# Performance work log

Hardware: AMD Instinct MI355X
Metric: run time of the kernel (lower is better)

The kernel has to match this reference:

```python
import jax, jax.numpy as jnp
import numpy as np

T, B, E, H = 2048, 2, 1024, 16
D = E // H  # head_dim = 64

def setup_inputs() -> dict:
    key = jax.random.key(0)
    ks = jax.random.split(key, 9)
    s = 1.0 / np.sqrt(E)
    return {
        "query": jax.random.normal(ks[0], (T, B, E), dtype=jnp.float32),
        "Wq": jax.random.normal(ks[1], (E, E), dtype=jnp.float32) * s,
        "bq": jax.random.normal(ks[2], (E,), dtype=jnp.float32) * 0.02,
        "Wk": jax.random.normal(ks[3], (E, E), dtype=jnp.float32) * s,
        "bk": jax.random.normal(ks[4], (E,), dtype=jnp.float32) * 0.02,
        "Wv": jax.random.normal(ks[5], (E, E), dtype=jnp.float32) * s,
        "bv": jax.random.normal(ks[6], (E,), dtype=jnp.float32) * 0.02,
        "Wo": jax.random.normal(ks[7], (E, E), dtype=jnp.float32) * s,
        "bo": jax.random.normal(ks[8], (E,), dtype=jnp.float32) * 0.02,
    }

def reference(query, Wq, bq, Wk, bk, Wv, bv, Wo, bo):
    # query: [T, B, E] (fairseq Time x Batch x Channel layout)
    t, b, e = query.shape
    scaling = D ** -0.5
    q = (query @ Wq.T + bq) * scaling          # [T,B,E], scaled like fairseq
    k = query @ Wk.T + bk                      # self-attention: k,v from query
    v = query @ Wv.T + bv
    # split heads: [T,B,H,D]
    q = q.reshape(t, b, H, D)
    k = k.reshape(t, b, H, D)
    v = v.reshape(t, b, H, D)
    # attn weights: [B,H,T(tgt),S(src)]
    scores = jnp.einsum("tbhd,sbhd->bhts", q, k)
    probs = jax.nn.softmax(scores, axis=-1)
    # attend: [T,B,H,D] -> [T,B,E]
    ctx = jnp.einsum("bhts,sbhd->tbhd", probs, v).reshape(t, b, e)
    return ctx @ Wo.T + bo                     # [T,B,E]
```

## Files before the change

### kernel.cpp

```cpp
#include <hip/hip_runtime.h>
#include <hip/hip_bf16.h>
#include <math.h>

#define TT 2048
#define BB 2
#define EE 1024
#define HH 16
#define DD 64
#define RR (TT*BB)

typedef __bf16 bf16x8 __attribute__((ext_vector_type(8)));
typedef float  floatx4 __attribute__((ext_vector_type(4)));

__device__ __forceinline__ unsigned short f2b(float f) {
    union { float f; unsigned u; } x{f};
    return (unsigned short)((x.u + 0x7FFFu + ((x.u >> 16) & 1u)) >> 16);
}
__device__ __forceinline__ float b2f_lo(unsigned u) {
    union { unsigned u; float f; } x{u << 16}; return x.f;
}
__device__ __forceinline__ float b2f_hi(unsigned u) {
    union { unsigned u; float f; } x{u & 0xffff0000u}; return x.f;
}

__device__ __forceinline__ float exp2_fast(float x) {
    return __builtin_amdgcn_exp2f(x);
}

typedef const __attribute__((address_space(1))) unsigned int as1_u32;
typedef __attribute__((address_space(3))) unsigned int as3_u32;
__device__ __forceinline__ void gload16(const void* g, void* l) {
    __builtin_amdgcn_global_load_lds((as1_u32*)g, (as3_u32*)l, 16, 0, 0);
}

#define SCALE_Q 0.18033688011112042f

__device__ __forceinline__ int swz(int r) {
    return (r & 7) ^ (((r >> 3) & 3) << 1);
}

__global__ __launch_bounds__(256)
void pack_bf16(const float* __restrict__ x,  const float* __restrict__ wq,
               const float* __restrict__ wk, const float* __restrict__ wv,
               const float* __restrict__ wo, unsigned short* __restrict__ base,
               unsigned short* __restrict__ wob)
{
    const size_t M4 = (size_t)4 << 20, M7 = (size_t)7 << 20;
    const size_t e0 = ((size_t)blockIdx.x * 256 + threadIdx.x) * 8;
    const float* src;
    unsigned short* dst;
    if (e0 < M4) {
        src = x + e0; dst = base + e0;
    } else if (e0 < M7) {
        const int seg = (int)((e0 >> 20) - 4);
        const float* wsrc[3] = {wq, wk, wv};
        src = wsrc[seg] + (e0 & ((1u << 20) - 1));
        dst = base + e0;
    } else {
        src = wo + (e0 - M7); dst = wob + (e0 - M7);
    }
    const float4 a = *(const float4*)src;
    const float4 b = *(const float4*)(src + 4);
    union { unsigned short u[8]; uint4 v; } p;
    p.u[0] = f2b(a.x); p.u[1] = f2b(a.y); p.u[2] = f2b(a.z); p.u[3] = f2b(a.w);
    p.u[4] = f2b(b.x); p.u[5] = f2b(b.y); p.u[6] = f2b(b.z); p.u[7] = f2b(b.w);
    *(uint4*)dst = p.v;
}

template<int MODE>
__global__ __launch_bounds__(256)
void gemm_mfma(const unsigned short* __restrict__ A,
               const unsigned short* __restrict__ Bw,
               const float* __restrict__ b0, const float* __restrict__ b1,
               const float* __restrict__ b2,
               void* __restrict__ out0, void* __restrict__ out1,
               void* __restrict__ out2)
{
    constexpr int BM = 128;
    constexpr int BN = (MODE == 0) ? 128 : 64;
    constexpr int MT = 4;
    constexpr int NT = (MODE == 0) ? 4 : 2;
    constexpr int RA = BM / 32;
    constexpr int RB = BN / 32;
    constexpr int SMEM = (MODE == 0) ? 34816 : 24576;
    __shared__ __align__(16) unsigned char smem[SMEM];
    unsigned short* ldsA = (unsigned short*)smem;
    unsigned short* ldsB = (unsigned short*)(smem + BM * 128);

    const int tid  = threadIdx.x;
    const int w    = tid >> 6;
    const int lane = tid & 63;
    const int quad = lane >> 4;
    const int l15  = lane & 15;
    const int wm   = w & 1;
    const int wn   = w >> 1;
    const int i0   = blockIdx.x * BM;
    const int j0   = blockIdx.y * BN;

    const unsigned short* ga[RA];
    const unsigned short* gb[RB];
    #pragma unroll
    for (int r = 0; r < RA; ++r) {
        const int slot = r * 256 + tid;
        const int row  = slot >> 3;
        const int gc   = (slot & 7) ^ swz(row);
        ga[r] = A + (size_t)(i0 + row) * EE + gc * 8;
    }
    #pragma unroll
    for (int r = 0; r < RB; ++r) {
        const int slot = r * 256 + tid;
        const int row  = slot >> 3;
        const int gc   = (slot & 7) ^ swz(row);
        gb[r] = Bw + (size_t)(j0 + row) * EE + gc * 8;
    }

    int ofsA[2][MT], ofsB[2][NT];
    #pragma unroll
    for (int mt = 0; mt < MT; ++mt) {
        const int row = wm * 64 + mt * 16 + l15;
        #pragma unroll
        for (int ks = 0; ks < 2; ++ks)
            ofsA[ks][mt] = row * 64 + (((ks * 4 + quad) ^ swz(row)) << 3);
    }
    #pragma unroll
    for (int nt = 0; nt < NT; ++nt) {
        const int col = wn * (BN / 2) + nt * 16 + l15;
        #pragma unroll
        for (int ks = 0; ks < 2; ++ks)
            ofsB[ks][nt] = col * 64 + (((ks * 4 + quad) ^ swz(col)) << 3);
    }

    floatx4 acc[MT][NT];
    #pragma unroll
    for (int mt = 0; mt < MT; ++mt)
        #pragma unroll
        for (int nt = 0; nt < NT; ++nt)
            acc[mt][nt] = (floatx4){0.f, 0.f, 0.f, 0.f};

    for (int kk = 0; kk < EE; kk += 64) {
        __syncthreads();
        #pragma unroll
        for (int r = 0; r < RA; ++r)
            gload16(ga[r] + kk, ldsA + (r * 256 + w * 64) * 8);
        #pragma unroll
        for (int r = 0; r < RB; ++r)
            gload16(gb[r] + kk, ldsB + (r * 256 + w * 64) * 8);
        __syncthreads();

        #pragma unroll
        for (int ks = 0; ks < 2; ++ks) {
            bf16x8 af[MT], bfr[NT];
            #pragma unroll
            for (int mt = 0; mt < MT; ++mt)
                af[mt] = __builtin_bit_cast(bf16x8, *(const uint4*)&ldsA[ofsA[ks][mt]]);
            #pragma unroll
            for (int nt = 0; nt < NT; ++nt)
                bfr[nt] = __builtin_bit_cast(bf16x8, *(const uint4*)&ldsB[ofsB[ks][nt]]);
            #pragma unroll
            for (int mt = 0; mt < MT; ++mt)
                #pragma unroll
                for (int nt = 0; nt < NT; ++nt)
                    acc[mt][nt] = __builtin_amdgcn_mfma_f32_16x16x32_bf16(
                        af[mt], bfr[nt], acc[mt][nt], 0, 0, 0);
        }
    }

    if (MODE == 1) {
        float* dst = (float*)out0;
        #pragma unroll
        for (int nt = 0; nt < NT; ++nt) {
            const int j = j0 + wn * 32 + nt * 16 + l15;
            const float bb = b0[j];
            #pragma unroll
            for (int mt = 0; mt < MT; ++mt) {
                const int i = i0 + wm * 64 + mt * 16 + quad * 4;
                #pragma unroll
                for (int r2 = 0; r2 < 4; ++r2)
                    dst[(size_t)(i + r2) * EE + j] = acc[mt][nt][r2] + bb;
            }
        }
    } else {
        const int which = j0 >> 10;
        const float scale = (which == 0) ? SCALE_Q : 1.0f;
        const float* bias = (which == 0) ? b0 : (which == 1) ? b1 : b2;
        if (which < 2) {
            unsigned short* dst = (unsigned short*)(which == 0 ? out0 : out1);
            #pragma unroll
            for (int nt = 0; nt < NT; ++nt) {
                const int j = (j0 & 1023) + wn * 64 + nt * 16 + l15;
                const int h = j >> 6, d = j & 63;
                const float bb = bias[j];
                #pragma unroll
                for (int mt = 0; mt < MT; ++mt) {
                    const int i = i0 + wm * 64 + mt * 16 + quad * 4;
                    #pragma unroll
                    for (int r2 = 0; r2 < 4; ++r2) {
                        const int ii = i + r2;
                        const int t = ii >> 1, b = ii & 1;
                        dst[((size_t)(b * HH + h) * TT + t) * DD + d] =
                            f2b((acc[mt][nt][r2] + bb) * scale);
                    }
                }
            }
        } else {
            __syncthreads();
            unsigned short* tr = (unsigned short*)smem + (size_t)w * 64 * 68;
            #pragma unroll
            for (int nt = 0; nt < NT; ++nt) {
                const int jl = nt * 16 + l15;
                const float bb = bias[(j0 & 1023) + wn * 64 + jl];
                #pragma unroll
                for (int mt = 0; mt < MT; ++mt) {
                    const int il0 = mt * 16 + quad * 4;
                    ushort4 h4;
                    h4.x = f2b(acc[mt][nt][0] + bb);
                    h4.y = f2b(acc[mt][nt][1] + bb);
                    h4.z = f2b(acc[mt][nt][2] + bb);
                    h4.w = f2b(acc[mt][nt][3] + bb);
                    *(ushort4*)&tr[jl * 68 + il0] = h4;
                }
            }
            __syncthreads();
            const int jg = (j0 & 1023) + wn * 64 + lane;
            const int h = jg >> 6, d = jg & 63;
            const int tb = (i0 + wm * 64) >> 1;
            const unsigned short* rp = tr + (size_t)lane * 68;
            unsigned short* dstV = (unsigned short*)out2;
            #pragma unroll
            for (int g = 0; g < 4; ++g) {
                union { unsigned short u[8]; uint4 v; } pe, po;
                #pragma unroll
                for (int k = 0; k < 8; ++k) {
                    pe.u[k] = rp[(g * 8 + k) * 2];
                    po.u[k] = rp[(g * 8 + k) * 2 + 1];
                }
                *(uint4*)&dstV[((size_t)(0 * HH + h) * DD + d) * TT + tb + g * 8] = pe.v;
                *(uint4*)&dstV[((size_t)(1 * HH + h) * DD + d) * TT + tb + g * 8] = po.v;
            }
        }
    }
}

__global__ __launch_bounds__(256)
void attn_mfma(const unsigned short* __restrict__ Q,
               const unsigned short* __restrict__ K,
               const unsigned short* __restrict__ Vt,
               unsigned short* __restrict__ cpart,
               float* __restrict__ lsumbuf)
{
    __shared__ __align__(16) unsigned short ksm[2][64 * 64];
    __shared__ __align__(16) unsigned short vtm[2][64 * 64];

    const int tid  = threadIdx.x;
    const int w    = tid >> 6;
    const int lane = tid & 63;
    const int quad = lane >> 4;
    const int l15  = lane & 15;
    const int bh   = blockIdx.x;
    const int tt   = blockIdx.y;
    const int half = blockIdx.z;

    const unsigned short* Qh = Q  + (size_t)bh * TT * DD;
    const unsigned short* Kh = K  + (size_t)bh * TT * DD;
    const unsigned short* Vh = Vt + (size_t)bh * DD * TT;

    const int q0w  = tt * 128 + w * 32;
    const int key0 = half * 1024;

    bf16x8 qf[2][2];
    #pragma unroll
    for (int qn = 0; qn < 2; ++qn)
        #pragma unroll
        for (int kd = 0; kd < 2; ++kd)
            qf[qn][kd] = __builtin_bit_cast(bf16x8,
                *(const uint4*)&Qh[(size_t)(q0w + qn * 16 + l15) * DD + kd * 32 + quad * 8]);

    const unsigned short* kg[4];
    #pragma unroll
    for (int r = 0; r < 4; ++r) {
        const int slot = r * 256 + tid;
        const int row  = slot >> 3;
        const int gc   = (slot & 7) ^ swz(row);
        kg[r] = Kh + (size_t)(key0 + row) * DD + gc * 8;
    }
    const unsigned short* vg[4];
    #pragma unroll
    for (int r = 0; r < 4; ++r) {
        const int s512 = (r & 1) * 256 + tid;
        const int rowd = s512 >> 3;
        const int gc   = (s512 & 7) ^ swz(rowd);
        vg[r] = Vh + (size_t)rowd * TT + key0 + (r >> 1) * 64 + gc * 8;
    }

    int ofsKA[4][2], ofsVB[4][2];
    #pragma unroll
    for (int mt = 0; mt < 4; ++mt) {
        const int row = ((mt >> 1) << 5) + ((l15 >> 2) << 3) + ((mt & 1) << 2) + (l15 & 3);
        #pragma unroll
        for (int kd = 0; kd < 2; ++kd)
            ofsKA[mt][kd] = row * 64 + (((kd * 4 + quad) ^ swz(row)) << 3);
    }
    #pragma unroll
    for (int dn = 0; dn < 4; ++dn) {
        const int row = dn * 16 + l15;
        #pragma unroll
        for (int ks = 0; ks < 2; ++ks)
            ofsVB[dn][ks] = row * 64 + (((ks * 4 + quad) ^ swz(row)) << 3);
    }

    floatx4 cacc[4][2];
    #pragma unroll
    for (int dn = 0; dn < 4; ++dn)
        #pragma unroll
        for (int qn = 0; qn < 2; ++qn)
            cacc[dn][qn] = (floatx4){0.f, 0.f, 0.f, 0.f};
    float rs[2] = {0.f, 0.f};

    for (int big = 0; big < 8; ++big) {
        const size_t ko = (size_t)big * 128;
        __syncthreads();
        gload16(kg[0] + ko * DD, &ksm[0][(size_t)(0 * 256 + w * 64) * 8]);
        gload16(kg[1] + ko * DD, &ksm[0][(size_t)(1 * 256 + w * 64) * 8]);
        gload16(kg[2] + ko * DD, &ksm[1][(size_t)(0 * 256 + w * 64) * 8]);
        gload16(kg[3] + ko * DD, &ksm[1][(size_t)(1 * 256 + w * 64) * 8]);
        gload16(vg[0] + ko,      &vtm[0][(size_t)(0 * 256 + w * 64) * 8]);
        gload16(vg[1] + ko,      &vtm[0][(size_t)(1 * 256 + w * 64) * 8]);
        gload16(vg[2] + ko,      &vtm[1][(size_t)(0 * 256 + w * 64) * 8]);
        gload16(vg[3] + ko,      &vtm[1][(size_t)(1 * 256 + w * 64) * 8]);
        __syncthreads();

        #pragma unroll
        for (int sub = 0; sub < 2; ++sub) {
            uint2 pk[4][2];
            #pragma unroll
            for (int mt = 0; mt < 4; ++mt) {
                const bf16x8 ka0 = __builtin_bit_cast(bf16x8, *(const uint4*)&ksm[sub][ofsKA[mt][0]]);
                const bf16x8 ka1 = __builtin_bit_cast(bf16x8, *(const uint4*)&ksm[sub][ofsKA[mt][1]]);
                #pragma unroll
                for (int qn = 0; qn < 2; ++qn) {
                    floatx4 s = (floatx4){0.f, 0.f, 0.f, 0.f};
                    s = __builtin_amdgcn_mfma_f32_16x16x32_bf16(ka0, qf[qn][0], s, 0, 0, 0);
                    s = __builtin_amdgcn_mfma_f32_16x16x32_bf16(ka1, qf[qn][1], s, 0, 0, 0);
                    const float p0 = exp2_fast(s[0]);
                    const float p1 = exp2_fast(s[1]);
                    const float p2 = exp2_fast(s[2]);
                    const float p3 = exp2_fast(s[3]);
                    rs[qn] += (p0 + p1) + (p2 + p3);
                    union { __hip_bfloat162 h2[2]; uint2 u; } c;
                    c.h2[0] = __float22bfloat162_rn(make_float2(p0, p1));
                    c.h2[1] = __float22bfloat162_rn(make_float2(p2, p3));
                    pk[mt][qn] = c.u;
                }
            }
            bf16x8 pa[2][2];
            #pragma unroll
            for (int qn = 0; qn < 2; ++qn) {
                union { uint2 d[2]; uint4 v; } a0, a1;
                a0.d[0] = pk[0][qn]; a0.d[1] = pk[1][qn];
                a1.d[0] = pk[2][qn]; a1.d[1] = pk[3][qn];
                pa[qn][0] = __builtin_bit_cast(bf16x8, a0.v);
                pa[qn][1] = __builtin_bit_cast(bf16x8, a1.v);
            }
            #pragma unroll
            for (int dn = 0; dn < 4; ++dn) {
                const bf16x8 vb0 = __builtin_bit_cast(bf16x8, *(const uint4*)&vtm[sub][ofsVB[dn][0]]);
                const bf16x8 vb1 = __builtin_bit_cast(bf16x8, *(const uint4*)&vtm[sub][ofsVB[dn][1]]);
                #pragma unroll
                for (int qn = 0; qn < 2; ++qn) {
                    cacc[dn][qn] = __builtin_amdgcn_mfma_f32_16x16x32_bf16(pa[qn][0], vb0, cacc[dn][qn], 0, 0, 0);
                    cacc[dn][qn] = __builtin_amdgcn_mfma_f32_16x16x32_bf16(pa[qn][1], vb1, cacc[dn][qn], 0, 0, 0);
                }
            }
        }
    }

    const int b = bh / HH, hh = bh % HH;
    float rsw[2];
    #pragma unroll
    for (int qn = 0; qn < 2; ++qn) {
        float t = rs[qn];
        t += __shfl_xor(t, 16);
        t += __shfl_xor(t, 32);
        rsw[qn] = t;
    }
    unsigned short* cp = cpart + (size_t)half * RR * EE;
    #pragma unroll
    for (int qn = 0; qn < 2; ++qn) {
        #pragma unroll
        for (int dn = 0; dn < 4; ++dn) {
            const int e = hh * 64 + dn * 16 + l15;
            #pragma unroll
            for (int j = 0; j < 4; ++j) {
                const int t = q0w + qn * 16 + quad * 4 + j;
                cp[(size_t)(t * BB + b) * EE + e] = f2b(cacc[dn][qn][j]);
            }
        }
    }
    if (quad == 0) {
        lsumbuf[(half * BB * HH + bh) * TT + q0w + 0 * 16 + l15] = rsw[0];
        lsumbuf[(half * BB * HH + bh) * TT + q0w + 1 * 16 + l15] = rsw[1];
    }
}

__global__ __launch_bounds__(256)
void combine(const unsigned short* __restrict__ cpart,
             const float* __restrict__ lsumbuf,
             unsigned short* __restrict__ cb)
{
    const int gid = blockIdx.x * 256 + threadIdx.x;
    const int e0 = (gid & 127) * 8;
    const int r  = gid >> 7;
    const int t = r >> 1, b = r & 1;
    const int h = e0 >> 6;
    const int bh = b * HH + h;
    const float inv = 1.0f /
        (lsumbuf[bh * TT + t] + lsumbuf[(BB * HH + bh) * TT + t]);
    const uint4 c0 = *(const uint4*)&cpart[(size_t)r * EE + e0];
    const uint4 c1 = *(const uint4*)&cpart[(size_t)RR * EE + (size_t)r * EE + e0];
    const unsigned u0[4] = {c0.x, c0.y, c0.z, c0.w};
    const unsigned u1[4] = {c1.x, c1.y, c1.z, c1.w};
    union { unsigned u[4]; uint4 v; } o;
    #pragma unroll
    for (int k = 0; k < 4; ++k) {
        const float lo = (b2f_lo(u0[k]) + b2f_lo(u1[k])) * inv;
        const float hi = (b2f_hi(u0[k]) + b2f_hi(u1[k])) * inv;
        union { __hip_bfloat162 h2; unsigned u; } pk;
        pk.h2 = __float22bfloat162_rn(make_float2(lo, hi));
        o.u[k] = pk.u;
    }
    *(uint4*)&cb[(size_t)r * EE + e0] = o.v;
}

extern "C" void kernel_launch(void* const* d_in, const int* in_sizes, int n_in,
                              void* d_out, int out_size, void* d_ws, size_t ws_size,
                              hipStream_t stream)
{
    const float* x  = (const float*)d_in[0];
    const float* Wq = (const float*)d_in[1];
    const float* bq = (const float*)d_in[2];
    const float* Wk = (const float*)d_in[3];
    const float* bk = (const float*)d_in[4];
    const float* Wv = (const float*)d_in[5];
    const float* bv = (const float*)d_in[6];
    const float* Wo = (const float*)d_in[7];
    const float* bo = (const float*)d_in[8];
    float* out = (float*)d_out;

    const size_t M1 = (size_t)1 << 20;
    unsigned short* base  = (unsigned short*)d_ws;
    unsigned short* xb    = base;
    unsigned short* wqkv  = base + 4 * M1;
    unsigned short* cpart = base;
    unsigned short* qb    = base + 8 * M1;
    unsigned short* kb    = base + 12 * M1;
    unsigned short* vtb   = base + 16 * M1;
    unsigned short* cb    = base + 20 * M1;
    unsigned short* wob   = base + 24 * M1;
    float*          lsum  = (float*)(base + 25 * M1);

    dim3 blk(256);

    pack_bf16<<<dim3(4096), blk, 0, stream>>>(x, Wq, Wk, Wv, Wo, base, wob);

    gemm_mfma<0><<<dim3(RR / 128, 3072 / 128), blk, 0, stream>>>(
        xb, wqkv, bq, bk, bv, qb, kb, vtb);

    attn_mfma<<<dim3(BB * HH, TT / 128, 2), blk, 0, stream>>>(qb, kb, vtb, cpart, lsum);

    combine<<<dim3(RR * EE / 8 / 256), blk, 0, stream>>>(cpart, lsum, cb);

    gemm_mfma<1><<<dim3(RR / 128, EE / 64), blk, 0, stream>>>(
        cb, wob, bo, nullptr, nullptr, out, nullptr, nullptr);
}
```

Before: 196.8 us.

## Use single-wave attention blocks with fp16 P·V and per-wave K/V tiles

The attention kernel now runs one 64-lane wave per block over 32 queries, loading 32-key K/V tiles into its own small LDS buffers. This removes the block-wide __syncthreads and replaces them with a vmcnt wait. V is now stored as fp16 by the QKV GEMM, and probabilities are packed with cvt_pkrtz so the P·V product uses the f16 MFMA. The goal is cheaper packing and more resident blocks without barriers. The cost is that each block no longer shares K/V loads across waves, which multiplies global/L2 traffic, and the smaller tiles add per-iteration overhead with no load double-buffering.

```diff
diff --git a/kernel.cpp b/kernel.cpp
--- a/kernel.cpp
+++ b/kernel.cpp
@@ -9,12 +9,18 @@
 #define DD 64
 #define RR (TT*BB)
 
-typedef __bf16 bf16x8 __attribute__((ext_vector_type(8)));
-typedef float  floatx4 __attribute__((ext_vector_type(4)));
+typedef __bf16    bf16x8  __attribute__((ext_vector_type(8)));
+typedef _Float16  halfx8  __attribute__((ext_vector_type(8)));
+typedef _Float16  halfx2  __attribute__((ext_vector_type(2)));
+typedef float     floatx4 __attribute__((ext_vector_type(4)));
 
 __device__ __forceinline__ unsigned short f2b(float f) {
     union { float f; unsigned u; } x{f};
     return (unsigned short)((x.u + 0x7FFFu + ((x.u >> 16) & 1u)) >> 16);
+}
+__device__ __forceinline__ unsigned short f2h(float f) {
+    union { _Float16 h; unsigned short u; } x{(_Float16)f};
+    return x.u;
 }
 __device__ __forceinline__ float b2f_lo(unsigned u) {
     union { unsigned u; float f; } x{u << 16}; return x.f;
@@ -213,10 +219,10 @@
                 for (int mt = 0; mt < MT; ++mt) {
                     const int il0 = mt * 16 + quad * 4;
                     ushort4 h4;
-                    h4.x = f2b(acc[mt][nt][0] + bb);
-                    h4.y = f2b(acc[mt][nt][1] + bb);
-                    h4.z = f2b(acc[mt][nt][2] + bb);
-                    h4.w = f2b(acc[mt][nt][3] + bb);
+                    h4.x = f2h(acc[mt][nt][0] + bb);
+                    h4.y = f2h(acc[mt][nt][1] + bb);
+                    h4.z = f2h(acc[mt][nt][2] + bb);
+                    h4.w = f2h(acc[mt][nt][3] + bb);
                     *(ushort4*)&tr[jl * 68 + il0] = h4;
                 }
             }
@@ -241,19 +247,17 @@
     }
 }
 
-__global__ __launch_bounds__(256)
+__global__ __launch_bounds__(64)
 void attn_mfma(const unsigned short* __restrict__ Q,
                const unsigned short* __restrict__ K,
                const unsigned short* __restrict__ Vt,
                unsigned short* __restrict__ cpart,
                float* __restrict__ lsumbuf)
 {
-    __shared__ __align__(16) unsigned short ksm[2][64 * 64];
-    __shared__ __align__(16) unsigned short vtm[2][64 * 64];
-
-    const int tid  = threadIdx.x;
-    const int w    = tid >> 6;
-    const int lane = tid & 63;
+    __shared__ __align__(16) unsigned short ksm[32 * 64];
+    __shared__ __align__(16) _Float16      vtm[64 * 32];
+
+    const int lane = threadIdx.x;
     const int quad = lane >> 4;
     const int l15  = lane & 15;
     const int bh   = blockIdx.x;
@@ -262,9 +266,9 @@
 
     const unsigned short* Qh = Q  + (size_t)bh * TT * DD;
     const unsigned short* Kh = K  + (size_t)bh * TT * DD;
-    const unsigned short* Vh = Vt + (size_t)bh * DD * TT;
-
-    const int q0w  = tt * 128 + w * 32;
+    const _Float16*       Vh = (const _Float16*)Vt + (size_t)bh * DD * TT;
+
+    const int q0w  = tt * 32;
     const int key0 = half * 1024;
 
     bf16x8 qf[2][2];
@@ -278,34 +282,32 @@
     const unsigned short* kg[4];
     #pragma unroll
     for (int r = 0; r < 4; ++r) {
-        const int slot = r * 256 + tid;
+        const int slot = r * 64 + lane;
         const int row  = slot >> 3;
-        const int gc   = (slot & 7) ^ swz(row);
+        const int gc   = (slot & 7) ^ (row & 7);
         kg[r] = Kh + (size_t)(key0 + row) * DD + gc * 8;
     }
-    const unsigned short* vg[4];
+    const _Float16* vg[4];
     #pragma unroll
     for (int r = 0; r < 4; ++r) {
-        const int s512 = (r & 1) * 256 + tid;
-        const int rowd = s512 >> 3;
-        const int gc   = (s512 & 7) ^ swz(rowd);
-        vg[r] = Vh + (size_t)rowd * TT + key0 + (r >> 1) * 64 + gc * 8;
-    }
-
-    int ofsKA[4][2], ofsVB[4][2];
-    #pragma unroll
-    for (int mt = 0; mt < 4; ++mt) {
-        const int row = ((mt >> 1) << 5) + ((l15 >> 2) << 3) + ((mt & 1) << 2) + (l15 & 3);
+        const int slot = r * 64 + lane;
+        const int row  = slot >> 2;
+        const int gc   = (slot & 3) ^ ((row >> 1) & 3);
+        vg[r] = Vh + (size_t)row * TT + key0 + gc * 8;
+    }
+
+    int ofsKA[2][2], ofsVB[4];
+    #pragma unroll
+    for (int mt = 0; mt < 2; ++mt) {
+        const int row = ((l15 >> 2) << 3) + (mt << 2) + (l15 & 3);
         #pragma unroll
         for (int kd = 0; kd < 2; ++kd)
-            ofsKA[mt][kd] = row * 64 + (((kd * 4 + quad) ^ swz(row)) << 3);
+            ofsKA[mt][kd] = row * 64 + (((kd * 4 + quad) ^ (row & 7)) << 3);
     }
     #pragma unroll
     for (int dn = 0; dn < 4; ++dn) {
         const int row = dn * 16 + l15;
-        #pragma unroll
-        for (int ks = 0; ks < 2; ++ks)
-            ofsVB[dn][ks] = row * 64 + (((ks * 4 + quad) ^ swz(row)) << 3);
+        ofsVB[dn] = row * 32 + ((quad ^ ((row >> 1) & 3)) << 3);
     }
 
     floatx4 cacc[4][2];
@@ -316,61 +318,49 @@
             cacc[dn][qn] = (floatx4){0.f, 0.f, 0.f, 0.f};
     float rs[2] = {0.f, 0.f};
 
-    for (int big = 0; big < 8; ++big) {
-        const size_t ko = (size_t)big * 128;
-        __syncthreads();
-        gload16(kg[0] + ko * DD, &ksm[0][(size_t)(0 * 256 + w * 64) * 8]);
-        gload16(kg[1] + ko * DD, &ksm[0][(size_t)(1 * 256 + w * 64) * 8]);
-        gload16(kg[2] + ko * DD, &ksm[1][(size_t)(0 * 256 + w * 64) * 8]);
-        gload16(kg[3] + ko * DD, &ksm[1][(size_t)(1 * 256 + w * 64) * 8]);
-        gload16(vg[0] + ko,      &vtm[0][(size_t)(0 * 256 + w * 64) * 8]);
-        gload16(vg[1] + ko,      &vtm[0][(size_t)(1 * 256 + w * 64) * 8]);
-        gload16(vg[2] + ko,      &vtm[1][(size_t)(0 * 256 + w * 64) * 8]);
-        gload16(vg[3] + ko,      &vtm[1][(size_t)(1 * 256 + w * 64) * 8]);
-        __syncthreads();
-
-        #pragma unroll
-        for (int sub = 0; sub < 2; ++sub) {
-            uint2 pk[4][2];
-            #pragma unroll
-            for (int mt = 0; mt < 4; ++mt) {
-                const bf16x8 ka0 = __builtin_bit_cast(bf16x8, *(const uint4*)&ksm[sub][ofsKA[mt][0]]);
-                const bf16x8 ka1 = __builtin_bit_cast(bf16x8, *(const uint4*)&ksm[sub][ofsKA[mt][1]]);
-                #pragma unroll
-                for (int qn = 0; qn < 2; ++qn) {
-                    floatx4 s = (floatx4){0.f, 0.f, 0.f, 0.f};
-                    s = __builtin_amdgcn_mfma_f32_16x16x32_bf16(ka0, qf[qn][0], s, 0, 0, 0);
-                    s = __builtin_amdgcn_mfma_f32_16x16x32_bf16(ka1, qf[qn][1], s, 0, 0, 0);
-                    const float p0 = exp2_fast(s[0]);
-                    const float p1 = exp2_fast(s[1]);
-                    const float p2 = exp2_fast(s[2]);
-                    const float p3 = exp2_fast(s[3]);
-                    rs[qn] += (p0 + p1) + (p2 + p3);
-                    union { __hip_bfloat162 h2[2]; uint2 u; } c;
-                    c.h2[0] = __float22bfloat162_rn(make_float2(p0, p1));
-                    c.h2[1] = __float22bfloat162_rn(make_float2(p2, p3));
-                    pk[mt][qn] = c.u;
-                }
-            }
-            bf16x8 pa[2][2];
+    for (int st = 0; st < 32; ++st) {
+        const size_t ko = (size_t)st * 32;
+        #pragma unroll
+        for (int r = 0; r < 4; ++r)
+            gload16(kg[r] + ko * DD, (unsigned short*)ksm + r * 512);
+        #pragma unroll
+        for (int r = 0; r < 4; ++r)
+            gload16(vg[r] + ko, (_Float16*)vtm + r * 512);
+        asm volatile("s_waitcnt vmcnt(0)" ::: "memory");
+
+        unsigned pk[2][2][2];
+        #pragma unroll
+        for (int mt = 0; mt < 2; ++mt) {
+            const bf16x8 ka0 = __builtin_bit_cast(bf16x8, *(const uint4*)&ksm[ofsKA[mt][0]]);
+            const bf16x8 ka1 = __builtin_bit_cast(bf16x8, *(const uint4*)&ksm[ofsKA[mt][1]]);
             #pragma unroll
             for (int qn = 0; qn < 2; ++qn) {
-                union { uint2 d[2]; uint4 v; } a0, a1;
-                a0.d[0] = pk[0][qn]; a0.d[1] = pk[1][qn];
-                a1.d[0] = pk[2][qn]; a1.d[1] = pk[3][qn];
-                pa[qn][0] = __builtin_bit_cast(bf16x8, a0.v);
-                pa[qn][1] = __builtin_bit_cast(bf16x8, a1.v);
-            }
-            #pragma unroll
-            for (int dn = 0; dn < 4; ++dn) {
-                const bf16x8 vb0 = __builtin_bit_cast(bf16x8, *(const uint4*)&vtm[sub][ofsVB[dn][0]]);
-                const bf16x8 vb1 = __builtin_bit_cast(bf16x8, *(const uint4*)&vtm[sub][ofsVB[dn][1]]);
-                #pragma unroll
-                for (int qn = 0; qn < 2; ++qn) {
-                    cacc[dn][qn] = __builtin_amdgcn_mfma_f32_16x16x32_bf16(pa[qn][0], vb0, cacc[dn][qn], 0, 0, 0);
-                    cacc[dn][qn] = __builtin_amdgcn_mfma_f32_16x16x32_bf16(pa[qn][1], vb1, cacc[dn][qn], 0, 0, 0);
-                }
-            }
+                floatx4 s = (floatx4){0.f, 0.f, 0.f, 0.f};
+                s = __builtin_amdgcn_mfma_f32_16x16x32_bf16(ka0, qf[qn][0], s, 0, 0, 0);
+                s = __builtin_amdgcn_mfma_f32_16x16x32_bf16(ka1, qf[qn][1], s, 0, 0, 0);
+                const float p0 = exp2_fast(s[0]);
+                const float p1 = exp2_fast(s[1]);
+                const float p2 = exp2_fast(s[2]);
+                const float p3 = exp2_fast(s[3]);
+                rs[qn] += (p0 + p1) + (p2 + p3);
+                pk[mt][qn][0] = __builtin_bit_cast(unsigned, __builtin_amdgcn_cvt_pkrtz(p0, p1));
+                pk[mt][qn][1] = __builtin_bit_cast(unsigned, __builtin_amdgcn_cvt_pkrtz(p2, p3));
+            }
+        }
+        halfx8 pa[2];
+        #pragma unroll
+        for (int qn = 0; qn < 2; ++qn) {
+            union { unsigned d[4]; uint4 v; } a;
+            a.d[0] = pk[0][qn][0]; a.d[1] = pk[0][qn][1];
+            a.d[2] = pk[1][qn][0]; a.d[3] = pk[1][qn][1];
+            pa[qn] = __builtin_bit_cast(halfx8, a.v);
+        }
+        #pragma unroll
+        for (int dn = 0; dn < 4; ++dn) {
+            const halfx8 vb = __builtin_bit_cast(halfx8, *(const uint4*)&vtm[ofsVB[dn]]);
+            #pragma unroll
+            for (int qn = 0; qn < 2; ++qn)
+                cacc[dn][qn] = __builtin_amdgcn_mfma_f32_16x16x32_f16(pa[qn], vb, cacc[dn][qn], 0, 0, 0);
         }
     }
 
@@ -465,7 +455,7 @@
     gemm_mfma<0><<<dim3(RR / 128, 3072 / 128), blk, 0, stream>>>(
         xb, wqkv, bq, bk, bv, qb, kb, vtb);
 
-    attn_mfma<<<dim3(BB * HH, TT / 128, 2), blk, 0, stream>>>(qb, kb, vtb, cpart, lsum);
+    attn_mfma<<<dim3(BB * HH, TT / 32, 2), dim3(64), 0, stream>>>(qb, kb, vtb, cpart, lsum);
 
     combine<<<dim3(RR * EE / 8 / 256), blk, 0, stream>>>(cpart, lsum, cb);
 
```

Measured after the change: 208.5 us. 1.06x slower.
